# Optimization experiments

Measured on AMD Instinct MI355X. Metric: run time of the kernel, lower is better.

## Reference

```python
import jax, jax.numpy as jnp
import numpy as np

B, S, D = 32, 577, 768
H, Dh = 12, 64  # num_attention_heads, attention_head_size = pruned_dim // heads


def setup_inputs() -> dict:
    key = jax.random.key(0)
    ks = jax.random.split(key, 7)
    s = 1.0 / np.sqrt(D)
    return {
        "hidden_states": jax.random.normal(ks[0], (B, S, D), dtype=jnp.float32),
        "Wq": jax.random.normal(ks[1], (D, H * Dh), dtype=jnp.float32) * s,
        "bq": jnp.zeros((H * Dh,), dtype=jnp.float32),
        "Wk": jax.random.normal(ks[2], (D, H * Dh), dtype=jnp.float32) * s,
        "bk": jnp.zeros((H * Dh,), dtype=jnp.float32),
        "Wv": jax.random.normal(ks[3], (D, H * Dh), dtype=jnp.float32) * s,
        "bv": jnp.zeros((H * Dh,), dtype=jnp.float32),
    }


def reference(hidden_states, Wq, bq, Wk, bk, Wv, bv):
    def heads(x):  # [B,S,H*Dh] -> [B,H,S,Dh]
        return x.reshape(B, S, H, Dh).transpose(0, 2, 1, 3)

    q = heads(hidden_states @ Wq + bq)
    k = heads(hidden_states @ Wk + bk)
    v = heads(hidden_states @ Wv + bv)

    scale = 1.0 / np.sqrt(Dh)
    scores = jnp.einsum("bhqd,bhkd->bhqk", q, k) * scale  # [B,H,S,S]
    probs = jax.nn.softmax(scores, axis=-1)  # dropout p=0.0 -> identity
    ctx = jnp.einsum("bhqk,bhkd->bhqd", probs, v)  # [B,H,S,Dh]
    ctx = ctx.transpose(0, 2, 1, 3).reshape(B, S, H * Dh)
    return ctx
```

## Files before the change

### kernel.cpp

```cpp
#include <hip/hip_runtime.h>

#define NB 32
#define SEQ 577
#define SP 640
#define DM 768
#define NH 12
#define DH 64
#define NC 10
#define CVT_XBLK 2048

typedef __attribute__((ext_vector_type(8))) short bf16x8;
typedef __attribute__((ext_vector_type(4))) short bf16x4;
typedef __attribute__((ext_vector_type(4))) float f32x4;
typedef __attribute__((ext_vector_type(2))) unsigned int u32x2;
typedef __attribute__((ext_vector_type(4))) unsigned int u32x4;
typedef unsigned short u16;

__device__ __forceinline__ u16 f2bf(float f) {
  unsigned int u = __builtin_bit_cast(unsigned int, f);
  u += 0x7fffu + ((u >> 16) & 1u);
  return (u16)(u >> 16);
}

__device__ __forceinline__ unsigned int pack_bf2(float a, float b) {
  unsigned int ua = __builtin_bit_cast(unsigned int, a) + 0x8000u;
  unsigned int ub = __builtin_bit_cast(unsigned int, b) + 0x8000u;
  return __builtin_amdgcn_perm(ub, ua, 0x07060302u);
}

__device__ __forceinline__ void g2l16(const void* g, void* lds) {
  __builtin_amdgcn_global_load_lds(
      (const __attribute__((address_space(1))) void*)g,
      (__attribute__((address_space(3))) void*)lds, 16, 0, 0);
}

__global__ __launch_bounds__(256)
void cvt_kernel(const float* __restrict__ X, u16* __restrict__ Xb,
                const float* __restrict__ Wq, const float* __restrict__ Wk,
                const float* __restrict__ Wv, u16* __restrict__ Wt) {
  __shared__ u16 ld[64 * 72];
  const int tid = threadIdx.x;
  if (blockIdx.x < CVT_XBLK) {
    const int n4 = 3545088;
    for (int i = blockIdx.x * 256 + tid; i < n4; i += CVT_XBLK * 256) {
      f32x4 v = *reinterpret_cast<const f32x4*>(X + (size_t)i * 4);
      u32x2 p;
      p[0] = pack_bf2(v[0], v[1]);
      p[1] = pack_bf2(v[2], v[3]);
      p[0] = (unsigned)f2bf(v[0]) | ((unsigned)f2bf(v[1]) << 16);
      p[1] = (unsigned)f2bf(v[2]) | ((unsigned)f2bf(v[3]) << 16);
      *reinterpret_cast<u32x2*>(Xb + (size_t)i * 4) = p;
    }
  } else {
    const int idx = blockIdx.x - CVT_XBLK;
    const int m = idx / 144;
    const int rem = idx - m * 144;
    const int by = rem / 12, bx = rem - by * 12;
    const int k0 = by * 64, n0 = bx * 64;
    const float* W = (m == 0) ? Wq : (m == 1) ? Wk : Wv;
    const int kr = tid >> 4, c4 = tid & 15;
#pragma unroll
    for (int p = 0; p < 4; ++p) {
      const int k = p * 16 + kr;
      f32x4 v = *reinterpret_cast<const f32x4*>(&W[(size_t)(k0 + k) * DM + n0 + c4 * 4]);
#pragma unroll
      for (int e = 0; e < 4; ++e) ld[(c4 * 4 + e) * 72 + k] = f2bf(v[e]);
    }
    __syncthreads();
    u16* dst = Wt + (size_t)m * DM * DM;
#pragma unroll
    for (int p = 0; p < 2; ++p) {
      const int s = p * 256 + tid;
      const int n = s >> 3, ch = (s & 7) * 8;
      u32x4 w = *reinterpret_cast<const u32x4*>(&ld[n * 72 + ch]);
      *reinterpret_cast<u32x4*>(&dst[(size_t)(n0 + n) * DM + k0 + ch]) = w;
    }
  }
}

__global__ __launch_bounds__(512, 2)
void qkv_gemm_kernel(const u16* __restrict__ Xb, const u16* __restrict__ Wt,
                     const float* __restrict__ bq, const float* __restrict__ bk,
                     const float* __restrict__ bv,
                     u16* __restrict__ Qw, u16* __restrict__ Kw, u16* __restrict__ Vw) {
  __shared__ alignas(16) u16 sh[256 * 264];

  const int tid = threadIdx.x;
  const int lane = tid & 63;
  const int wid = tid >> 6;
  const int wm = wid >> 2, wn = wid & 3;
  const int l15 = lane & 15, lq = lane >> 4;

  const int flat = (blockIdx.z * 3 + blockIdx.y) * 80 + blockIdx.x;
  const int xcd = flat & 7;
  const int j8 = flat >> 3;
  const int xi = j8 / 9;
  const int yz = j8 - xi * 9;
  const int mt = xi * 8 + xcd;
  const int nt = yz % 3;
  const int qkv = yz / 3;

  const u16* Wm = Wt + (size_t)qkv * DM * DM;
  const float* bias = (qkv == 0) ? bq : (qkv == 1) ? bk : bv;

  const u16* gA[2];
  const u16* gB[2];
#pragma unroll
  for (int s = 0; s < 2; ++s) {
    const int e = wid * 2 + s;
    int r = mt * 256 + e * 16 + l15;
    int br = r / SP;
    int tr = r - br * SP;
    if (tr >= SEQ) tr = SEQ - 1;
    gA[s] = Xb + (size_t)(br * SEQ + tr) * DM + lq * 8;
    gB[s] = Wm + (size_t)(nt * 256 + e * 16 + l15) * DM + lq * 8;
  }

  f32x4 acc[8][4];
#pragma unroll
  for (int i = 0; i < 8; ++i)
#pragma unroll
    for (int j = 0; j < 4; ++j)
#pragma unroll
      for (int r = 0; r < 4; ++r) acc[i][j][r] = 0.0f;

  auto stageA = [&](int buf, int kt) {
    g2l16(gA[0] + kt * 32, &sh[buf * 8192 + (wid * 2 + 0) * 512]);
    g2l16(gA[1] + kt * 32, &sh[buf * 8192 + (wid * 2 + 1) * 512]);
  };
  auto stageB = [&](int buf, int kt) {
    g2l16(gB[0] + kt * 32, &sh[32768 + buf * 8192 + (wid * 2 + 0) * 512]);
    g2l16(gB[1] + kt * 32, &sh[32768 + buf * 8192 + (wid * 2 + 1) * 512]);
  };

  stageA(0, 0); stageB(0, 0);
  stageA(1, 1); stageB(1, 1);
  stageA(2, 2); stageB(2, 2);
  asm volatile("s_waitcnt vmcnt(8)" ::: "memory");
  __builtin_amdgcn_s_barrier();

  const int NKT = DM / 32;
#pragma unroll
  for (int kt = 0; kt < NKT; ++kt) {
    const int buf = kt & 3;
    const int nbuf = (kt + 3) & 3;
    const bool more = (kt + 3 < NKT);
    bf16x8 af[8], bf4[4];

#pragma unroll
    for (int i = 0; i < 8; ++i)
      af[i] = *reinterpret_cast<const bf16x8*>(&sh[buf * 8192 + ((wm * 8 + i) * 64 + lane) * 8]);
#pragma unroll
    for (int j = 0; j < 4; ++j)
      bf4[j] = *reinterpret_cast<const bf16x8*>(&sh[32768 + buf * 8192 + ((wn * 4 + j) * 64 + lane) * 8]);

    if (more) { stageA(nbuf, kt + 3); stageB(nbuf, kt + 3); }

    if (kt <= NKT - 4) {
      asm volatile("s_waitcnt vmcnt(8)" ::: "memory");
    } else if (kt == NKT - 3) {
      asm volatile("s_waitcnt vmcnt(4)" ::: "memory");
    } else if (kt == NKT - 2) {
      asm volatile("s_waitcnt vmcnt(0)" ::: "memory");
    }
    __builtin_amdgcn_s_barrier();

    __builtin_amdgcn_s_setprio(1);
#pragma unroll
    for (int i = 0; i < 8; ++i)
#pragma unroll
      for (int j = 0; j < 4; ++j)
        acc[i][j] = __builtin_amdgcn_mfma_f32_16x16x32_bf16(af[i], bf4[j], acc[i][j], 0, 0, 0);
    __builtin_amdgcn_s_setprio(0);
    __builtin_amdgcn_s_barrier();
  }

  const float sfold = 0.18033688011112042f;
#pragma unroll
  for (int j = 0; j < 4; ++j) {
    const int col = wn * 64 + j * 16 + l15;
    const float bb = bias[nt * 256 + col];
#pragma unroll
    for (int i = 0; i < 8; ++i) {
      const int row = wm * 128 + i * 16 + lq * 4;
      if (qkv == 2) {
        unsigned p0 = (unsigned)f2bf(acc[i][j][0] + bb) | ((unsigned)f2bf(acc[i][j][1] + bb) << 16);
        unsigned p1 = (unsigned)f2bf(acc[i][j][2] + bb) | ((unsigned)f2bf(acc[i][j][3] + bb) << 16);
        *reinterpret_cast<u32x2*>(&sh[col * 264 + row]) = u32x2{p0, p1};
      } else {
#pragma unroll
        for (int r = 0; r < 4; ++r) {
          float v = acc[i][j][r] + bb;
          if (qkv == 0) v *= sfold;
          sh[(row + r) * 264 + col] = f2bf(v);
        }
      }
    }
  }
  __builtin_amdgcn_s_barrier();

#pragma unroll
  for (int p = 0; p < 16; ++p) {
    const int slot = p * 512 + tid;
    const int rr = slot >> 5;
    const int cc = (slot & 31) * 8;
    u32x4 w = *reinterpret_cast<const u32x4*>(&sh[rr * 264 + cc]);
    if (qkv == 2) {
      const int gcol = nt * 256 + rr;
      const int h = gcol >> 6, d = gcol & 63;
      const int rg = mt * 256 + cc;
      const int br = rg / SP, tr = rg - br * SP;
      *reinterpret_cast<u32x4*>(&Vw[((size_t)(br * NH + h) * DH + d) * SP + tr]) = w;
    } else {
      const int rg = mt * 256 + rr;
      const int br = rg / SP, tr = rg - br * SP;
      const int gcol = nt * 256 + cc;
      const int h = gcol >> 6, d = gcol & 63;
      u16* dst = ((qkv == 0) ? Qw : Kw) + ((size_t)(br * NH + h) * SP + tr) * DH + d;
      *reinterpret_cast<u32x4*>(dst) = w;
    }
  }
}

#if __has_builtin(__builtin_amdgcn_mfma_f32_16x16x16bf16_1k)
#define MFMA16(a, b, c) __builtin_amdgcn_mfma_f32_16x16x16bf16_1k(a, b, c, 0, 0, 0)
#define HAVE_MFMA16 1
#elif __has_builtin(__builtin_amdgcn_mfma_f32_16x16x16_bf16)
#define MFMA16(a, b, c) __builtin_amdgcn_mfma_f32_16x16x16_bf16(a, b, c, 0, 0, 0)
#define HAVE_MFMA16 1
#else
#define HAVE_MFMA16 0
#endif

__global__ __launch_bounds__(256)
void attn_kernel(const u16* __restrict__ Qw, const u16* __restrict__ Kw,
                 const u16* __restrict__ Vw, float* __restrict__ out) {
  __shared__ alignas(16) u16 Kc[2][8 * 64 * 8];
  __shared__ alignas(16) u16 Vc[2][16 * 64 * 4];

  const int tid = threadIdx.x;
  const int lane = tid & 63;
  const int wid = tid >> 6;
  const int l15 = lane & 15, lq = lane >> 4;

  const int flat = blockIdx.y * 5 + blockIdx.x;
  const int w = (flat & 7) * 240 + (flat >> 3);
  const int qx = w % 5;
  const int bh = w / 5;
  const int b = bh / NH;
  const int h = bh - b * NH;
  const int q0 = qx * 128 + wid * 32;

  const u16* Qb = Qw + (size_t)bh * SP * DH;
  const u16* Kb = Kw + (size_t)bh * SP * DH;
  const u16* Vb = Vw + (size_t)bh * DH * SP;

  bf16x8 qf[2][2];
#pragma unroll
  for (int qt = 0; qt < 2; ++qt)
#pragma unroll
    for (int hf = 0; hf < 2; ++hf)
      qf[qt][hf] = *reinterpret_cast<const bf16x8*>(
          &Qb[(q0 + qt * 16 + l15) * DH + hf * 32 + lq * 8]);

  const u16* gK = Kb + (size_t)(wid * 16 + l15) * DH + lq * 8;
  const u16* gV = Vb + (size_t)(wid * 16 + l15) * SP + lq * 4;

  float mrow[2] = {-__builtin_inff(), -__builtin_inff()};
  float lrow[2] = {0.0f, 0.0f};
  f32x4 acc[2][4];
#pragma unroll
  for (int qt = 0; qt < 2; ++qt)
#pragma unroll
    for (int dt = 0; dt < 4; ++dt)
#pragma unroll
      for (int r = 0; r < 4; ++r) acc[qt][dt][r] = 0.0f;

  g2l16(gK, &Kc[0][(wid * 2 + 0) * 512]);
  g2l16(gK + 32, &Kc[0][(wid * 2 + 1) * 512]);
  {
    u32x2 v[4];
#pragma unroll
    for (int t = 0; t < 4; ++t)
      v[t] = *reinterpret_cast<const u32x2*>(gV + t * 16);
#pragma unroll
    for (int t = 0; t < 4; ++t)
      *reinterpret_cast<u32x2*>(&Vc[0][((wid * 4 + t) * 64 + lane) * 4]) = v[t];
  }
  __syncthreads();

  for (int c = 0; c < NC; ++c) {
    const int cur = c & 1;
    const int c0 = c * 64;
    u32x2 vn[4];
    if (c + 1 < NC) {
      const u16* gKn = gK + (size_t)(c0 + 64) * DH;
      g2l16(gKn, &Kc[cur ^ 1][(wid * 2 + 0) * 512]);
      g2l16(gKn + 32, &Kc[cur ^ 1][(wid * 2 + 1) * 512]);
#pragma unroll
      for (int t = 0; t < 4; ++t)
        vn[t] = *reinterpret_cast<const u32x2*>(gV + (c0 + 64) + t * 16);
    }

    f32x4 s[2][4];
    __builtin_amdgcn_s_setprio(1);
#pragma unroll
    for (int t = 0; t < 4; ++t) {
      bf16x8 kf0 = *reinterpret_cast<const bf16x8*>(&Kc[cur][((t * 2 + 0) * 64 + lane) * 8]);
      bf16x8 kf1 = *reinterpret_cast<const bf16x8*>(&Kc[cur][((t * 2 + 1) * 64 + lane) * 8]);
#pragma unroll
      for (int qt = 0; qt < 2; ++qt) {
        f32x4 z;
#pragma unroll
        for (int r = 0; r < 4; ++r) z[r] = 0.0f;
        z = __builtin_amdgcn_mfma_f32_16x16x32_bf16(kf0, qf[qt][0], z, 0, 0, 0);
        z = __builtin_amdgcn_mfma_f32_16x16x32_bf16(kf1, qf[qt][1], z, 0, 0, 0);
        s[qt][t] = z;
      }
    }
    __builtin_amdgcn_s_setprio(0);
    if (c0 + 64 > SEQ) {
#pragma unroll
      for (int qt = 0; qt < 2; ++qt)
#pragma unroll
        for (int t = 0; t < 4; ++t)
#pragma unroll
          for (int r = 0; r < 4; ++r) {
            int key = c0 + t * 16 + lq * 4 + r;
            s[qt][t][r] = (key < SEQ) ? s[qt][t][r] : -__builtin_inff();
          }
    }
    float alpha[2];
    unsigned int pku[2][4][2];
#pragma unroll
    for (int qt = 0; qt < 2; ++qt) {
      float mx = s[qt][0][0];
#pragma unroll
      for (int t = 0; t < 4; ++t)
#pragma unroll
        for (int r = 0; r < 4; ++r) mx = fmaxf(mx, s[qt][t][r]);
      mx = fmaxf(mx, __shfl_xor(mx, 16));
      mx = fmaxf(mx, __shfl_xor(mx, 32));
      float mn = fmaxf(mrow[qt], mx);
      alpha[qt] = __builtin_amdgcn_exp2f(mrow[qt] - mn);
      mrow[qt] = mn;
      float sm = 0.0f;
#pragma unroll
      for (int t = 0; t < 4; ++t) {
        float p0 = __builtin_amdgcn_exp2f(s[qt][t][0] - mn);
        float p1 = __builtin_amdgcn_exp2f(s[qt][t][1] - mn);
        float p2 = __builtin_amdgcn_exp2f(s[qt][t][2] - mn);
        float p3 = __builtin_amdgcn_exp2f(s[qt][t][3] - mn);
        sm += (p0 + p1) + (p2 + p3);
        pku[qt][t][0] = pack_bf2(p0, p1);
        pku[qt][t][1] = pack_bf2(p2, p3);
      }
      sm += __shfl_xor(sm, 16);
      sm += __shfl_xor(sm, 32);
      lrow[qt] = lrow[qt] * alpha[qt] + sm;
    }

#if HAVE_MFMA16
    __builtin_amdgcn_s_setprio(1);
#pragma unroll
    for (int dt = 0; dt < 4; ++dt) {
      bf16x4 vf[4];
#pragma unroll
      for (int t = 0; t < 4; ++t)
        vf[t] = *reinterpret_cast<const bf16x4*>(&Vc[cur][((dt * 4 + t) * 64 + lane) * 4]);
#pragma unroll
      for (int qt = 0; qt < 2; ++qt) {
        f32x4 a = acc[qt][dt];
#pragma unroll
        for (int r = 0; r < 4; ++r) a[r] *= alpha[qt];
#pragma unroll
        for (int t = 0; t < 4; ++t) {
          bf16x4 pf = __builtin_bit_cast(bf16x4, u32x2{pku[qt][t][0], pku[qt][t][1]});
          a = MFMA16(vf[t], pf, a);
        }
        acc[qt][dt] = a;
      }
    }
    __builtin_amdgcn_s_setprio(0);
#else
#pragma unroll
    for (int qt = 0; qt < 2; ++qt) {
      unsigned int bfrag[2][4];
#pragma unroll
      for (int hh = 0; hh < 2; ++hh)
#pragma unroll
        for (int w2 = 0; w2 < 4; ++w2) {
          int srcl = l15 + 16 * (2 * (lq & 1) + (w2 >> 1));
          unsigned int lo = (unsigned int)__shfl((int)pku[qt][2 * hh][w2 & 1], srcl);
          unsigned int hi = (unsigned int)__shfl((int)pku[qt][2 * hh + 1][w2 & 1], srcl);
          bfrag[hh][w2] = (lq < 2) ? lo : hi;
        }
#pragma unroll
      for (int dt = 0; dt < 4; ++dt) {
        f32x4 a = acc[qt][dt];
#pragma unroll
        for (int r = 0; r < 4; ++r) a[r] *= alpha[qt];
#pragma unroll
        for (int hh = 0; hh < 2; ++hh) {
          u32x2 w0 = *reinterpret_cast<const u32x2*>(&Vc[cur][((dt * 4 + 2 * hh) * 64 + lane) * 4]);
          u32x2 w1 = *reinterpret_cast<const u32x2*>(&Vc[cur][((dt * 4 + 2 * hh + 1) * 64 + lane) * 4]);
          u32x4 vw = {w0[0], w0[1], w1[0], w1[1]};
          u32x4 pw = {bfrag[hh][0], bfrag[hh][1], bfrag[hh][2], bfrag[hh][3]};
          a = __builtin_amdgcn_mfma_f32_16x16x32_bf16(
              __builtin_bit_cast(bf16x8, vw), __builtin_bit_cast(bf16x8, pw), a, 0, 0, 0);
        }
        acc[qt][dt] = a;
      }
    }
#endif

    if (c + 1 < NC) {
#pragma unroll
      for (int t = 0; t < 4; ++t)
        *reinterpret_cast<u32x2*>(&Vc[cur ^ 1][((wid * 4 + t) * 64 + lane) * 4]) = vn[t];
    }
    __syncthreads();
  }

#pragma unroll
  for (int qt = 0; qt < 2; ++qt) {
    int q = q0 + qt * 16 + l15;
    if (q < SEQ) {
      float rl = 1.0f / lrow[qt];
      float* orow = out + ((size_t)b * SEQ + q) * DM + h * DH;
#pragma unroll
      for (int dt = 0; dt < 4; ++dt) {
        f32x4 v = acc[qt][dt];
#pragma unroll
        for (int r = 0; r < 4; ++r) v[r] *= rl;
        *reinterpret_cast<f32x4*>(&orow[dt * 16 + lq * 4]) = v;
      }
    }
  }
}

extern "C" void kernel_launch(void* const* d_in, const int* in_sizes, int n_in,
                              void* d_out, int out_size, void* d_ws, size_t ws_size,
                              hipStream_t stream) {
  (void)in_sizes; (void)n_in; (void)out_size; (void)ws_size;
  const float* X  = (const float*)d_in[0];
  const float* Wq = (const float*)d_in[1];
  const float* bq = (const float*)d_in[2];
  const float* Wk = (const float*)d_in[3];
  const float* bk = (const float*)d_in[4];
  const float* Wv = (const float*)d_in[5];
  const float* bv = (const float*)d_in[6];
  float* out = (float*)d_out;

  char* ws = (char*)d_ws;
  u16* Xb = (u16*)ws;
  u16* Wt = (u16*)(ws + 28366848);
  u16* Qw = (u16*)(ws + 28366848 + 3538944);
  u16* Kw = Qw + (size_t)NB * NH * SP * DH;
  u16* Vw = Kw + (size_t)NB * NH * SP * DH;

  cvt_kernel<<<dim3(CVT_XBLK + 432), 256, 0, stream>>>(X, Xb, Wq, Wk, Wv, Wt);
  qkv_gemm_kernel<<<dim3(80, 3, 3), 512, 0, stream>>>(Xb, Wt, bq, bk, bv, Qw, Kw, Vw);
  attn_kernel<<<dim3(5, NB * NH), 256, 0, stream>>>(Qw, Kw, Vw, out);
}
```

Baseline: 298.7 us.

## Shrink QKV GEMM tiles to 128x128 with double-buffered LDS pipeline

The QKV projection GEMM moves from 256x256 tiles with 512 threads and a 4-stage global-to-LDS pipeline to 128x128 tiles with 256 threads, two LDS buffers, and up to three blocks per CU. The grid grows to 160x6x3. Tiles now align to per-batch 128-row chunks of the padded sequence, so the row-to-batch division goes away. The aim is more blocks for occupancy and load balance, at the cost of less data reuse per tile and a shallower prefetch, with a full vmcnt(0) wait every iteration. A redundant pack in the conversion kernel is also removed.

New measurement: 338.3 us. 1.13x slower.

```diff
diff --git a/kernel.cpp b/kernel.cpp
--- a/kernel.cpp
+++ b/kernel.cpp
@@ -45,8 +45,6 @@
     for (int i = blockIdx.x * 256 + tid; i < n4; i += CVT_XBLK * 256) {
       f32x4 v = *reinterpret_cast<const f32x4*>(X + (size_t)i * 4);
       u32x2 p;
-      p[0] = pack_bf2(v[0], v[1]);
-      p[1] = pack_bf2(v[2], v[3]);
       p[0] = (unsigned)f2bf(v[0]) | ((unsigned)f2bf(v[1]) << 16);
       p[1] = (unsigned)f2bf(v[2]) | ((unsigned)f2bf(v[3]) << 16);
       *reinterpret_cast<u32x2*>(Xb + (size_t)i * 4) = p;
@@ -78,27 +76,30 @@
   }
 }
 
-__global__ __launch_bounds__(512, 2)
+__global__ __launch_bounds__(256, 3)
 void qkv_gemm_kernel(const u16* __restrict__ Xb, const u16* __restrict__ Wt,
                      const float* __restrict__ bq, const float* __restrict__ bk,
                      const float* __restrict__ bv,
                      u16* __restrict__ Qw, u16* __restrict__ Kw, u16* __restrict__ Vw) {
-  __shared__ alignas(16) u16 sh[256 * 264];
+  __shared__ alignas(16) u16 sh[128 * 136];
 
   const int tid = threadIdx.x;
   const int lane = tid & 63;
   const int wid = tid >> 6;
-  const int wm = wid >> 2, wn = wid & 3;
+  const int wm = wid >> 1, wn = wid & 1;
   const int l15 = lane & 15, lq = lane >> 4;
 
-  const int flat = (blockIdx.z * 3 + blockIdx.y) * 80 + blockIdx.x;
+  const int flat = (blockIdx.z * 6 + blockIdx.y) * 160 + blockIdx.x;
   const int xcd = flat & 7;
   const int j8 = flat >> 3;
-  const int xi = j8 / 9;
-  const int yz = j8 - xi * 9;
+  const int xi = j8 / 18;
+  const int yz = j8 - xi * 18;
   const int mt = xi * 8 + xcd;
-  const int nt = yz % 3;
-  const int qkv = yz / 3;
+  const int nt = yz % 6;
+  const int qkv = yz / 6;
+
+  const int b = mt / 5;
+  const int t0 = (mt - b * 5) * 128;
 
   const u16* Wm = Wt + (size_t)qkv * DM * DM;
   const float* bias = (qkv == 0) ? bq : (qkv == 1) ? bk : bv;
@@ -108,70 +109,58 @@
 #pragma unroll
   for (int s = 0; s < 2; ++s) {
     const int e = wid * 2 + s;
-    int r = mt * 256 + e * 16 + l15;
-    int br = r / SP;
-    int tr = r - br * SP;
+    int tr = t0 + e * 16 + l15;
     if (tr >= SEQ) tr = SEQ - 1;
-    gA[s] = Xb + (size_t)(br * SEQ + tr) * DM + lq * 8;
-    gB[s] = Wm + (size_t)(nt * 256 + e * 16 + l15) * DM + lq * 8;
-  }
-
-  f32x4 acc[8][4];
-#pragma unroll
-  for (int i = 0; i < 8; ++i)
+    gA[s] = Xb + (size_t)(b * SEQ + tr) * DM + lq * 8;
+    gB[s] = Wm + (size_t)(nt * 128 + e * 16 + l15) * DM + lq * 8;
+  }
+
+  f32x4 acc[4][4];
+#pragma unroll
+  for (int i = 0; i < 4; ++i)
 #pragma unroll
     for (int j = 0; j < 4; ++j)
 #pragma unroll
       for (int r = 0; r < 4; ++r) acc[i][j][r] = 0.0f;
 
   auto stageA = [&](int buf, int kt) {
-    g2l16(gA[0] + kt * 32, &sh[buf * 8192 + (wid * 2 + 0) * 512]);
-    g2l16(gA[1] + kt * 32, &sh[buf * 8192 + (wid * 2 + 1) * 512]);
+    g2l16(gA[0] + kt * 32, &sh[buf * 4096 + (wid * 2 + 0) * 512]);
+    g2l16(gA[1] + kt * 32, &sh[buf * 4096 + (wid * 2 + 1) * 512]);
   };
   auto stageB = [&](int buf, int kt) {
-    g2l16(gB[0] + kt * 32, &sh[32768 + buf * 8192 + (wid * 2 + 0) * 512]);
-    g2l16(gB[1] + kt * 32, &sh[32768 + buf * 8192 + (wid * 2 + 1) * 512]);
+    g2l16(gB[0] + kt * 32, &sh[8192 + buf * 4096 + (wid * 2 + 0) * 512]);
+    g2l16(gB[1] + kt * 32, &sh[8192 + buf * 4096 + (wid * 2 + 1) * 512]);
   };
 
   stageA(0, 0); stageB(0, 0);
-  stageA(1, 1); stageB(1, 1);
-  stageA(2, 2); stageB(2, 2);
-  asm volatile("s_waitcnt vmcnt(8)" ::: "memory");
+  asm volatile("s_waitcnt vmcnt(0)" ::: "memory");
   __builtin_amdgcn_s_barrier();
 
   const int NKT = DM / 32;
 #pragma unroll
   for (int kt = 0; kt < NKT; ++kt) {
-    const int buf = kt & 3;
-    const int nbuf = (kt + 3) & 3;
-    const bool more = (kt + 3 < NKT);
-    bf16x8 af[8], bf4[4];
-
-#pragma unroll
-    for (int i = 0; i < 8; ++i)
-      af[i] = *reinterpret_cast<const bf16x8*>(&sh[buf * 8192 + ((wm * 8 + i) * 64 + lane) * 8]);
+    const int cur = kt & 1;
+    const bool more = (kt + 1 < NKT);
+
+    if (more) { stageA(cur ^ 1, kt + 1); stageB(cur ^ 1, kt + 1); }
+
+    bf16x8 af[4], bf[4];
+#pragma unroll
+    for (int i = 0; i < 4; ++i)
+      af[i] = *reinterpret_cast<const bf16x8*>(&sh[cur * 4096 + ((wm * 4 + i) * 64 + lane) * 8]);
 #pragma unroll
     for (int j = 0; j < 4; ++j)
-      bf4[j] = *reinterpret_cast<const bf16x8*>(&sh[32768 + buf * 8192 + ((wn * 4 + j) * 64 + lane) * 8]);
-
-    if (more) { stageA(nbuf, kt + 3); stageB(nbuf, kt + 3); }
-
-    if (kt <= NKT - 4) {
-      asm volatile("s_waitcnt vmcnt(8)" ::: "memory");
-    } else if (kt == NKT - 3) {
-      asm volatile("s_waitcnt vmcnt(4)" ::: "memory");
-    } else if (kt == NKT - 2) {
-      asm volatile("s_waitcnt vmcnt(0)" ::: "memory");
-    }
-    __builtin_amdgcn_s_barrier();
+      bf[j] = *reinterpret_cast<const bf16x8*>(&sh[8192 + cur * 4096 + ((wn * 4 + j) * 64 + lane) * 8]);
 
     __builtin_amdgcn_s_setprio(1);
 #pragma unroll
-    for (int i = 0; i < 8; ++i)
+    for (int i = 0; i < 4; ++i)
 #pragma unroll
       for (int j = 0; j < 4; ++j)
-        acc[i][j] = __builtin_amdgcn_mfma_f32_16x16x32_bf16(af[i], bf4[j], acc[i][j], 0, 0, 0);
+        acc[i][j] = __builtin_amdgcn_mfma_f32_16x16x32_bf16(af[i], bf[j], acc[i][j], 0, 0, 0);
     __builtin_amdgcn_s_setprio(0);
+
+    if (more) asm volatile("s_waitcnt vmcnt(0)" ::: "memory");
     __builtin_amdgcn_s_barrier();
   }
 
@@ -179,20 +168,20 @@
 #pragma unroll
   for (int j = 0; j < 4; ++j) {
     const int col = wn * 64 + j * 16 + l15;
-    const float bb = bias[nt * 256 + col];
-#pragma unroll
-    for (int i = 0; i < 8; ++i) {
-      const int row = wm * 128 + i * 16 + lq * 4;
+    const float bb = bias[nt * 128 + col];
+#pragma unroll
+    for (int i = 0; i < 4; ++i) {
+      const int rl = wm * 64 + i * 16 + lq * 4;
       if (qkv == 2) {
         unsigned p0 = (unsigned)f2bf(acc[i][j][0] + bb) | ((unsigned)f2bf(acc[i][j][1] + bb) << 16);
         unsigned p1 = (unsigned)f2bf(acc[i][j][2] + bb) | ((unsigned)f2bf(acc[i][j][3] + bb) << 16);
-        *reinterpret_cast<u32x2*>(&sh[col * 264 + row]) = u32x2{p0, p1};
+        *reinterpret_cast<u32x2*>(&sh[col * 136 + rl]) = u32x2{p0, p1};
       } else {
 #pragma unroll
         for (int r = 0; r < 4; ++r) {
           float v = acc[i][j][r] + bb;
           if (qkv == 0) v *= sfold;
-          sh[(row + r) * 264 + col] = f2bf(v);
+          sh[(rl + r) * 136 + col] = f2bf(v);
         }
       }
     }
@@ -200,23 +189,21 @@
   __builtin_amdgcn_s_barrier();
 
 #pragma unroll
-  for (int p = 0; p < 16; ++p) {
-    const int slot = p * 512 + tid;
-    const int rr = slot >> 5;
-    const int cc = (slot & 31) * 8;
-    u32x4 w = *reinterpret_cast<const u32x4*>(&sh[rr * 264 + cc]);
+  for (int pp = 0; pp < 8; ++pp) {
+    const int slot = pp * 256 + tid;
+    const int rr = slot >> 4;
+    const int cc = (slot & 15) * 8;
+    u32x4 w = *reinterpret_cast<const u32x4*>(&sh[rr * 136 + cc]);
     if (qkv == 2) {
-      const int gcol = nt * 256 + rr;
+      const int gcol = nt * 128 + rr;
       const int h = gcol >> 6, d = gcol & 63;
-      const int rg = mt * 256 + cc;
-      const int br = rg / SP, tr = rg - br * SP;
-      *reinterpret_cast<u32x4*>(&Vw[((size_t)(br * NH + h) * DH + d) * SP + tr]) = w;
+      const int tr = t0 + cc;
+      *reinterpret_cast<u32x4*>(&Vw[((size_t)(b * NH + h) * DH + d) * SP + tr]) = w;
     } else {
-      const int rg = mt * 256 + rr;
-      const int br = rg / SP, tr = rg - br * SP;
-      const int gcol = nt * 256 + cc;
+      const int tr = t0 + rr;
+      const int gcol = nt * 128 + cc;
       const int h = gcol >> 6, d = gcol & 63;
-      u16* dst = ((qkv == 0) ? Qw : Kw) + ((size_t)(br * NH + h) * SP + tr) * DH + d;
+      u16* dst = ((qkv == 0) ? Qw : Kw) + ((size_t)(b * NH + h) * SP + tr) * DH + d;
       *reinterpret_cast<u32x4*>(dst) = w;
     }
   }
@@ -460,6 +447,6 @@
   u16* Vw = Kw + (size_t)NB * NH * SP * DH;
 
   cvt_kernel<<<dim3(CVT_XBLK + 432), 256, 0, stream>>>(X, Xb, Wq, Wk, Wv, Wt);
-  qkv_gemm_kernel<<<dim3(80, 3, 3), 512, 0, stream>>>(Xb, Wt, bq, bk, bv, Qw, Kw, Vw);
+  qkv_gemm_kernel<<<dim3(160, 6, 3), 256, 0, stream>>>(Xb, Wt, bq, bk, bv, Qw, Kw, Vw);
   attn_kernel<<<dim3(5, NB * NH), 256, 0, stream>>>(Qw, Kw, Vw, out);
 }
```
